# Kernel tuning notes

Measured on AMD Instinct MI355X. Metric: run time of the kernel, lower is better.

The kernel has to match this reference:

```python
import jax, jax.numpy as jnp
import numpy as np

G, IN_D, OUT_D, KQ_D = 8192, 512, 512, 128
EPS = 1e-12  # torch F.normalize default eps


def setup_inputs() -> dict:
    key = jax.random.key(0)
    ks = jax.random.split(key, 7)
    s_in = 1.0 / np.sqrt(IN_D)
    return {
        "x": jax.random.normal(ks[0], (G, IN_D), dtype=jnp.float32),
        "Wk": jax.random.uniform(ks[1], (KQ_D, IN_D), jnp.float32, -s_in, s_in),
        "bk": jax.random.uniform(ks[2], (KQ_D,), jnp.float32, -s_in, s_in),
        "Wq": jax.random.uniform(ks[3], (KQ_D, IN_D), jnp.float32, -s_in, s_in),
        "bq": jax.random.uniform(ks[4], (KQ_D,), jnp.float32, -s_in, s_in),
        "Wv": jax.random.uniform(ks[5], (OUT_D, IN_D), jnp.float32, -s_in, s_in),
        "bv": jax.random.uniform(ks[6], (OUT_D,), jnp.float32, -s_in, s_in),
    }


def reference(x, Wk, bk, Wq, bq, Wv, bv):
    # QKV projections (torch Linear: x @ W^T + b)
    k = x @ Wk.T + bk            # [g, kq]
    q = x @ Wq.T + bq            # [g, kq]
    v = x @ Wv.T + bv            # [g, outD]
    # g x g attention scores
    scores = k @ q.T             # [g, g]
    # L2-normalize each row (F.normalize with dim=-1): x / max(||x||_2, eps)
    norm = jnp.sqrt(jnp.sum(scores * scores, axis=-1, keepdims=True))
    scores_n = scores / jnp.maximum(norm, EPS)
    # value matmul + residual
    return scores_n @ v + v      # [g, outD]
```

## Files before the change

### kernel.cpp

```cpp
#include <hip/hip_runtime.h>
#include <hip/hip_bf16.h>
#include <stdint.h>

typedef __attribute__((ext_vector_type(8))) short bf16x8;
typedef __attribute__((ext_vector_type(4))) float f32x4;

__device__ __forceinline__ unsigned short f2bf(float f) {
  union { float f; uint32_t u; } v; v.f = f;
  uint32_t u = v.u;
  return (unsigned short)((u + 0x7fffu + ((u >> 16) & 1u)) >> 16);
}
__device__ __forceinline__ float bf2f(unsigned short h) {
  union { uint32_t u; float f; } v; v.u = ((uint32_t)h) << 16;
  return v.f;
}

#define GLL(g, l) __builtin_amdgcn_global_load_lds( \
    (const __attribute__((address_space(1))) void*)(g), \
    (__attribute__((address_space(3))) void*)(l), 16, 0, 0)
#define WAITV(N) asm volatile("s_waitcnt vmcnt(" #N ")" ::: "memory")
#define SFENCE() __builtin_amdgcn_sched_barrier(0)
#define RBAR()   __builtin_amdgcn_s_barrier()

__global__ void cvt_all(const float* __restrict__ x,
                        const float* __restrict__ wk, const float* __restrict__ wq,
                        const float* __restrict__ wv,
                        unsigned short* __restrict__ xb, unsigned short* __restrict__ wb) {
  const int i = (blockIdx.x * 256 + threadIdx.x) * 4;
  const float* src; unsigned short* dst; int off;
  if (i < 4194304) { src = x; dst = xb; off = i; }
  else {
    const int j = i - 4194304;
    if (j < 65536)       { src = wk; off = j; }
    else if (j < 131072) { src = wq; off = j - 65536; }
    else                 { src = wv; off = j - 131072; }
    dst = wb + (j - off);
  }
  const float4 v = *(const float4*)(src + off);
  ushort4 o; o.x = f2bf(v.x); o.y = f2bf(v.y); o.z = f2bf(v.z); o.w = f2bf(v.w);
  *(ushort4*)(dst + off) = o;
}

__global__ __launch_bounds__(512, 2) void qkv_gemm(
    const unsigned short* __restrict__ xb, const unsigned short* __restrict__ wb,
    const float* __restrict__ pbk, const float* __restrict__ pbq, const float* __restrict__ pbv,
    unsigned short* __restrict__ kb, unsigned short* __restrict__ qtb,
    unsigned short* __restrict__ vb, unsigned short* __restrict__ vtb)
{
  __shared__ unsigned short Alds[2][128 * 64];
  __shared__ unsigned short Blds[2][192 * 64];
  const int tid = threadIdx.x;
  const int lane = tid & 63;
  const int wid = tid >> 6;
  const int wm = wid >> 2, wn = wid & 3;
  const int wg = blockIdx.x;
  const int s = (wg & 7) * 32 + (wg >> 3);
  const int m0 = (s & 63) * 128;
  const int n0 = (s >> 6) * 192;
  const int l15 = lane & 15, l4 = lane >> 4;

  f32x4 acc[4][3] = {};

  auto stage = [&](int b, int kt) {
    const int k0 = kt * 64;
    #pragma unroll
    for (int p = 0; p < 2; ++p) {
      const int e = p * 512 + tid;
      const int row = e >> 3;
      const int cs = (e & 7) ^ (row & 7);
      GLL(xb + (size_t)(m0 + row) * 512 + k0 + cs * 8, &Alds[b][(p * 512 + (tid & ~63)) * 8]);
    }
    #pragma unroll
    for (int p = 0; p < 3; ++p) {
      const int e = p * 512 + tid;
      const int row = e >> 3;
      const int cs = (e & 7) ^ (row & 7);
      GLL(wb + (size_t)(n0 + row) * 512 + k0 + cs * 8, &Blds[b][(p * 512 + (tid & ~63)) * 8]);
    }
  };

  stage(0, 0);
  stage(1, 1);

  for (int kt = 0; kt < 8; ++kt) {
    const int cur = kt & 1;
    if (kt < 7) { WAITV(5); } else { WAITV(0); }
    RBAR();
    SFENCE();
    #pragma unroll
    for (int kk = 0; kk < 2; ++kk) {
      bf16x8 af[4], bfv[3];
      const int c = kk * 4 + l4;
      #pragma unroll
      for (int i = 0; i < 4; ++i) {
        const int ra = wm * 64 + i * 16 + l15;
        af[i] = *(const bf16x8*)(&Alds[cur][ra * 64 + ((c ^ (ra & 7)) * 8)]);
      }
      #pragma unroll
      for (int j = 0; j < 3; ++j) {
        const int rb = wn * 48 + j * 16 + l15;
        bfv[j] = *(const bf16x8*)(&Blds[cur][rb * 64 + ((c ^ (rb & 7)) * 8)]);
      }
      #pragma unroll
      for (int i = 0; i < 4; ++i)
        #pragma unroll
        for (int j = 0; j < 3; ++j)
          acc[i][j] = __builtin_amdgcn_mfma_f32_16x16x32_bf16(af[i], bfv[j], acc[i][j], 0, 0, 0);
    }
    SFENCE();
    RBAR();
    if (kt < 6) stage(cur, kt + 2);
  }

  #pragma unroll
  for (int i = 0; i < 4; ++i) {
    #pragma unroll
    for (int j = 0; j < 3; ++j) {
      const int rbase = m0 + wm * 64 + i * 16 + l4 * 4;
      const int c = n0 + wn * 48 + j * 16 + l15;
      const float bias = (c < 128) ? pbk[c] : (c < 256) ? pbq[c - 128] : pbv[c - 256];
      unsigned short o[4];
      #pragma unroll
      for (int r = 0; r < 4; ++r) o[r] = f2bf(acc[i][j][r] + bias);
      if (c < 128) {
        #pragma unroll
        for (int r = 0; r < 4; ++r) kb[(size_t)(rbase + r) * 128 + c] = o[r];
      } else if (c < 256) {
        ushort4 t; t.x = o[0]; t.y = o[1]; t.z = o[2]; t.w = o[3];
        *(ushort4*)(qtb + (size_t)(c - 128) * 8192 + rbase) = t;
      } else {
        const int vcol = c - 256;
        #pragma unroll
        for (int r = 0; r < 4; ++r) vb[(size_t)(rbase + r) * 512 + vcol] = o[r];
        ushort4 t; t.x = o[0]; t.y = o[1]; t.z = o[2]; t.w = o[3];
        *(ushort4*)(vtb + (size_t)vcol * 8192 + rbase) = t;
      }
    }
  }
}

__global__ __launch_bounds__(512) void gh_gemm(
    const unsigned short* __restrict__ qtb, const unsigned short* __restrict__ vtb,
    unsigned short* __restrict__ pb)
{
  __shared__ unsigned short Alds[2][128 * 64];
  __shared__ unsigned short Blds[2][80 * 64];
  const int tid = threadIdx.x, lane = tid & 63, wid = tid >> 6;
  const int l15 = lane & 15, l4 = lane >> 4;
  const int kc = blockIdx.x, nq = blockIdx.y;
  const int g0 = kc * 256;
  const int m0 = wid * 16;

  f32x4 acc[5] = {};

  auto stage = [&](int b, int st) {
    const int gs = g0 + st * 64;
    #pragma unroll
    for (int p = 0; p < 2; ++p) {
      const int e = p * 512 + tid;
      const int row = e >> 3;
      const int cs = (e & 7) ^ (row & 7);
      GLL(qtb + (size_t)row * 8192 + gs + cs * 8, &Alds[b][(p * 512 + (tid & ~63)) * 8]);
    }
    {
      const int row = tid >> 3;
      const int cglob = nq * 80 + row;
      const unsigned short* src = (cglob < 128) ? (qtb + (size_t)cglob * 8192)
                                                : (vtb + (size_t)(cglob - 128) * 8192);
      const int cs = (tid & 7) ^ (row & 7);
      GLL(src + gs + cs * 8, &Blds[b][(tid & ~63) * 8]);
    }
    if (tid < 128) {
      const int e = 512 + tid;
      const int row = e >> 3;
      const int cglob = nq * 80 + row;
      const unsigned short* src = (cglob < 128) ? (qtb + (size_t)cglob * 8192)
                                                : (vtb + (size_t)(cglob - 128) * 8192);
      const int cs = (e & 7) ^ (row & 7);
      GLL(src + gs + cs * 8, &Blds[b][(512 + (tid & ~63)) * 8]);
    }
  };

  stage(0, 0);
  stage(1, 1);

  for (int st = 0; st < 4; ++st) {
    const int cur = st & 1;
    if (st < 3) { WAITV(3); } else { WAITV(0); }
    RBAR();
    SFENCE();
    #pragma unroll
    for (int ks = 0; ks < 2; ++ks) {
      const int ra = m0 + l15;
      const int ca = ks * 4 + l4;
      const bf16x8 af = *(const bf16x8*)(&Alds[cur][ra * 64 + ((ca ^ (ra & 7)) * 8)]);
      #pragma unroll
      for (int nf = 0; nf < 5; ++nf) {
        const int rb = nf * 16 + l15;
        const bf16x8 bf = *(const bf16x8*)(&Blds[cur][rb * 64 + ((ca ^ (rb & 7)) * 8)]);
        acc[nf] = __builtin_amdgcn_mfma_f32_16x16x32_bf16(af, bf, acc[nf], 0, 0, 0);
      }
    }
    SFENCE();
    RBAR();
    if (st < 2) stage(cur, st + 2);
  }

  #pragma unroll
  for (int nf = 0; nf < 5; ++nf) {
    const int col = nq * 80 + nf * 16 + l15;
    #pragma unroll
    for (int r = 0; r < 4; ++r) {
      const int row = m0 + l4 * 4 + r;
      pb[((size_t)kc * 128 + row) * 640 + col] = f2bf(acc[nf][r]);
    }
  }
}

__global__ void gh_finalize(const unsigned short* __restrict__ pb,
                            unsigned short* __restrict__ Gb, unsigned short* __restrict__ Hbt) {
  const int idx = blockIdx.x * 256 + threadIdx.x;
  float s = 0.f;
  #pragma unroll
  for (int p = 0; p < 32; ++p) s += bf2f(pb[(size_t)p * 81920 + idx]);
  const int m = idx / 640, c = idx % 640;
  if (c < 128) Gb[m * 128 + c] = f2bf(s);
  else         Hbt[(size_t)(c - 128) * 128 + m] = f2bf(s);
}

__global__ __launch_bounds__(512) void tnorm_uv(
    const unsigned short* __restrict__ kb, const unsigned short* __restrict__ Gb,
    const unsigned short* __restrict__ Hbt, const unsigned short* __restrict__ vb,
    float* __restrict__ out)
{
  __shared__ float ssq_part[8][16];
  __shared__ float rnorm_lds[16];
  const int tid = threadIdx.x, lane = tid & 63, wid = tid >> 6;
  const int l15 = lane & 15, l4 = lane >> 4;
  const int rowbase = blockIdx.x * 16;

  bf16x8 af[4];
  #pragma unroll
  for (int ks = 0; ks < 4; ++ks)
    af[ks] = *(const bf16x8*)(kb + (size_t)(rowbase + l15) * 128 + ks * 32 + l4 * 8);

  f32x4 tac = {};
  #pragma unroll
  for (int ks = 0; ks < 4; ++ks) {
    const bf16x8 bf = *(const bf16x8*)(Gb + (size_t)(wid * 16 + l15) * 128 + ks * 32 + l4 * 8);
    tac = __builtin_amdgcn_mfma_f32_16x16x32_bf16(af[ks], bf, tac, 0, 0, 0);
  }
  float ssq[4];
  #pragma unroll
  for (int r = 0; r < 4; ++r) {
    const int row = rowbase + l4 * 4 + r;
    ssq[r] = tac[r] * bf2f(kb[(size_t)row * 128 + wid * 16 + l15]);
  }
  #pragma unroll
  for (int d = 1; d < 16; d <<= 1)
    #pragma unroll
    for (int r = 0; r < 4; ++r) ssq[r] += __shfl_xor(ssq[r], d);
  if (l15 == 0) {
    #pragma unroll
    for (int r = 0; r < 4; ++r) ssq_part[wid][l4 * 4 + r] = ssq[r];
  }

  f32x4 acc[4] = {};
  #pragma unroll
  for (int ks = 0; ks < 4; ++ks) {
    #pragma unroll
    for (int nf = 0; nf < 4; ++nf) {
      const int col = wid * 64 + nf * 16 + l15;
      const bf16x8 bf = *(const bf16x8*)(Hbt + (size_t)col * 128 + ks * 32 + l4 * 8);
      acc[nf] = __builtin_amdgcn_mfma_f32_16x16x32_bf16(af[ks], bf, acc[nf], 0, 0, 0);
    }
  }
  float vres[4][4];
  #pragma unroll
  for (int nf = 0; nf < 4; ++nf) {
    const int col = wid * 64 + nf * 16 + l15;
    #pragma unroll
    for (int r = 0; r < 4; ++r)
      vres[nf][r] = bf2f(vb[(size_t)(rowbase + l4 * 4 + r) * 512 + col]);
  }

  __syncthreads();
  if (tid < 16) {
    float s = 0.f;
    #pragma unroll
    for (int w = 0; w < 8; ++w) s += ssq_part[w][tid];
    rnorm_lds[tid] = 1.0f / fmaxf(sqrtf(s), 1e-12f);
  }
  __syncthreads();

  float rn[4];
  #pragma unroll
  for (int r = 0; r < 4; ++r) rn[r] = rnorm_lds[l4 * 4 + r];

  #pragma unroll
  for (int nf = 0; nf < 4; ++nf) {
    const int col = wid * 64 + nf * 16 + l15;
    #pragma unroll
    for (int r = 0; r < 4; ++r) {
      const int row = rowbase + l4 * 4 + r;
      out[(size_t)row * 512 + col] = acc[nf][r] * rn[r] + vres[nf][r];
    }
  }
}

extern "C" void kernel_launch(void* const* d_in, const int* in_sizes, int n_in,
                              void* d_out, int out_size, void* d_ws, size_t ws_size,
                              hipStream_t stream) {
  const float* x  = (const float*)d_in[0];
  const float* Wk = (const float*)d_in[1];
  const float* bk = (const float*)d_in[2];
  const float* Wq = (const float*)d_in[3];
  const float* bq = (const float*)d_in[4];
  const float* Wv = (const float*)d_in[5];
  const float* bv = (const float*)d_in[6];
  float* out = (float*)d_out;

  char* ws = (char*)d_ws;
  unsigned short* xb   = (unsigned short*)(ws);
  unsigned short* wb   = (unsigned short*)(ws + 8388608);
  unsigned short* kb   = (unsigned short*)(ws + 9175040);
  unsigned short* vb   = (unsigned short*)(ws + 11272192);
  unsigned short* vtb  = (unsigned short*)(ws + 19660800);
  unsigned short* qtb  = (unsigned short*)(ws + 28049408);
  unsigned short* pb   = (unsigned short*)(ws + 30146560);
  unsigned short* Gb   = (unsigned short*)(ws + 35389440);
  unsigned short* Hbt  = (unsigned short*)(ws + 35422208);

  cvt_all<<<4480, 256, 0, stream>>>(x, Wk, Wq, Wv, xb, wb);
  qkv_gemm<<<256, 512, 0, stream>>>(xb, wb, bk, bq, bv, kb, qtb, vb, vtb);
  gh_gemm<<<dim3(32, 8), 512, 0, stream>>>(qtb, vtb, pb);
  gh_finalize<<<320, 256, 0, stream>>>(pb, Gb, Hbt);
  tnorm_uv<<<512, 512, 0, stream>>>(kb, Gb, Hbt, vb, out);
}
```

Measured before the change: 54.99 us.

## Retile QKV GEMM to 256-thread blocks and stage H into LDS

The QKV projection GEMM moves from 512-thread 128x192 tiles to 256-thread 128x96 tiles, doubling the grid and changing the XCD-aware block mapping. The final normalize-and-multiply kernel now handles 32 rows per block and loads the full 512x128 H^T matrix plus the K tile into swizzled LDS with async global-to-LDS loads, so each block reuses H^T from LDS instead of reading it from global memory per 16-row block. The aim is to cut redundant global traffic and improve occupancy balance. The trade-off is a large LDS footprint (about 136 KB) that limits tnorm_uv to one block per CU, plus an initial load latency per block.

After: 58.79 us. 1.07x slower.

```diff
diff --git a/kernel.cpp b/kernel.cpp
--- a/kernel.cpp
+++ b/kernel.cpp
@@ -41,22 +41,22 @@
   *(ushort4*)(dst + off) = o;
 }
 
-__global__ __launch_bounds__(512, 2) void qkv_gemm(
+__global__ __launch_bounds__(256, 2) void qkv_gemm(
     const unsigned short* __restrict__ xb, const unsigned short* __restrict__ wb,
     const float* __restrict__ pbk, const float* __restrict__ pbq, const float* __restrict__ pbv,
     unsigned short* __restrict__ kb, unsigned short* __restrict__ qtb,
     unsigned short* __restrict__ vb, unsigned short* __restrict__ vtb)
 {
   __shared__ unsigned short Alds[2][128 * 64];
-  __shared__ unsigned short Blds[2][192 * 64];
+  __shared__ unsigned short Blds[2][96 * 64];
   const int tid = threadIdx.x;
   const int lane = tid & 63;
   const int wid = tid >> 6;
-  const int wm = wid >> 2, wn = wid & 3;
+  const int wm = wid >> 1, wn = wid & 1;
   const int wg = blockIdx.x;
-  const int s = (wg & 7) * 32 + (wg >> 3);
-  const int m0 = (s & 63) * 128;
-  const int n0 = (s >> 6) * 192;
+  const int xcd = wg & 7, i6 = wg >> 3;
+  const int m0 = (xcd * 8 + (i6 & 7)) * 128;
+  const int n0 = (i6 >> 3) * 96;
   const int l15 = lane & 15, l4 = lane >> 4;
 
   f32x4 acc[4][3] = {};
@@ -64,18 +64,18 @@
   auto stage = [&](int b, int kt) {
     const int k0 = kt * 64;
     #pragma unroll
-    for (int p = 0; p < 2; ++p) {
-      const int e = p * 512 + tid;
+    for (int p = 0; p < 4; ++p) {
+      const int e = p * 256 + tid;
       const int row = e >> 3;
       const int cs = (e & 7) ^ (row & 7);
-      GLL(xb + (size_t)(m0 + row) * 512 + k0 + cs * 8, &Alds[b][(p * 512 + (tid & ~63)) * 8]);
+      GLL(xb + (size_t)(m0 + row) * 512 + k0 + cs * 8, &Alds[b][(p * 256 + (tid & ~63)) * 8]);
     }
     #pragma unroll
     for (int p = 0; p < 3; ++p) {
-      const int e = p * 512 + tid;
+      const int e = p * 256 + tid;
       const int row = e >> 3;
       const int cs = (e & 7) ^ (row & 7);
-      GLL(wb + (size_t)(n0 + row) * 512 + k0 + cs * 8, &Blds[b][(p * 512 + (tid & ~63)) * 8]);
+      GLL(wb + (size_t)(n0 + row) * 512 + k0 + cs * 8, &Blds[b][(p * 256 + (tid & ~63)) * 8]);
     }
   };
 
@@ -84,7 +84,7 @@
 
   for (int kt = 0; kt < 8; ++kt) {
     const int cur = kt & 1;
-    if (kt < 7) { WAITV(5); } else { WAITV(0); }
+    if (kt < 7) { WAITV(7); } else { WAITV(0); }
     RBAR();
     SFENCE();
     #pragma unroll
@@ -228,81 +228,115 @@
   else         Hbt[(size_t)(c - 128) * 128 + m] = f2bf(s);
 }
 
-__global__ __launch_bounds__(512) void tnorm_uv(
+__global__ __launch_bounds__(512, 1) void tnorm_uv(
     const unsigned short* __restrict__ kb, const unsigned short* __restrict__ Gb,
     const unsigned short* __restrict__ Hbt, const unsigned short* __restrict__ vb,
     float* __restrict__ out)
 {
-  __shared__ float ssq_part[8][16];
-  __shared__ float rnorm_lds[16];
+  __shared__ unsigned short Hlds[512 * 128];
+  __shared__ unsigned short Kld[32 * 128];
+  __shared__ float ssq_part[8][32];
+  __shared__ float rnorm_lds[32];
   const int tid = threadIdx.x, lane = tid & 63, wid = tid >> 6;
   const int l15 = lane & 15, l4 = lane >> 4;
-  const int rowbase = blockIdx.x * 16;
-
-  bf16x8 af[4];
-  #pragma unroll
-  for (int ks = 0; ks < 4; ++ks)
-    af[ks] = *(const bf16x8*)(kb + (size_t)(rowbase + l15) * 128 + ks * 32 + l4 * 8);
-
-  f32x4 tac = {};
+  const int m0 = blockIdx.x * 32;
+  const int mf = wid & 1, nq = wid >> 1;
+
+  {
+    const int row = tid >> 4, ch = tid & 15;
+    GLL(kb + (size_t)(m0 + row) * 128 + (ch ^ ((row & 7) << 1)) * 8,
+        &Kld[(tid & ~63) * 8]);
+  }
+  #pragma unroll
+  for (int p = 0; p < 16; ++p) {
+    const int e = p * 512 + tid;
+    const int row = e >> 4, ch = e & 15;
+    GLL(Hbt + (size_t)row * 128 + (ch ^ ((row & 7) << 1)) * 8,
+        &Hlds[(p * 512 + (tid & ~63)) * 8]);
+  }
+  WAITV(16);
+  __syncthreads();
+
+  bf16x8 afh[2][4];
+  #pragma unroll
+  for (int h = 0; h < 2; ++h)
+    #pragma unroll
+    for (int ks = 0; ks < 4; ++ks) {
+      const int row = h * 16 + l15, ci = ks * 4 + l4;
+      afh[h][ks] = *(const bf16x8*)((const char*)Kld + row * 256 + ((ci ^ ((row & 7) << 1)) * 16));
+    }
+  f32x4 tach[2] = {};
   #pragma unroll
   for (int ks = 0; ks < 4; ++ks) {
-    const bf16x8 bf = *(const bf16x8*)(Gb + (size_t)(wid * 16 + l15) * 128 + ks * 32 + l4 * 8);
-    tac = __builtin_amdgcn_mfma_f32_16x16x32_bf16(af[ks], bf, tac, 0, 0, 0);
-  }
-  float ssq[4];
-  #pragma unroll
-  for (int r = 0; r < 4; ++r) {
-    const int row = rowbase + l4 * 4 + r;
-    ssq[r] = tac[r] * bf2f(kb[(size_t)row * 128 + wid * 16 + l15]);
-  }
-  #pragma unroll
-  for (int d = 1; d < 16; d <<= 1)
-    #pragma unroll
-    for (int r = 0; r < 4; ++r) ssq[r] += __shfl_xor(ssq[r], d);
-  if (l15 == 0) {
-    #pragma unroll
-    for (int r = 0; r < 4; ++r) ssq_part[wid][l4 * 4 + r] = ssq[r];
-  }
-
-  f32x4 acc[4] = {};
-  #pragma unroll
-  for (int ks = 0; ks < 4; ++ks) {
-    #pragma unroll
-    for (int nf = 0; nf < 4; ++nf) {
-      const int col = wid * 64 + nf * 16 + l15;
-      const bf16x8 bf = *(const bf16x8*)(Hbt + (size_t)col * 128 + ks * 32 + l4 * 8);
-      acc[nf] = __builtin_amdgcn_mfma_f32_16x16x32_bf16(af[ks], bf, acc[nf], 0, 0, 0);
-    }
-  }
-  float vres[4][4];
-  #pragma unroll
-  for (int nf = 0; nf < 4; ++nf) {
-    const int col = wid * 64 + nf * 16 + l15;
-    #pragma unroll
-    for (int r = 0; r < 4; ++r)
-      vres[nf][r] = bf2f(vb[(size_t)(rowbase + l4 * 4 + r) * 512 + col]);
-  }
-
+    const bf16x8 bfG = *(const bf16x8*)(Gb + (size_t)(wid * 16 + l15) * 128 + ks * 32 + l4 * 8);
+    #pragma unroll
+    for (int h = 0; h < 2; ++h)
+      tach[h] = __builtin_amdgcn_mfma_f32_16x16x32_bf16(afh[h][ks], bfG, tach[h], 0, 0, 0);
+  }
+  #pragma unroll
+  for (int h = 0; h < 2; ++h) {
+    float ssq[4];
+    #pragma unroll
+    for (int r = 0; r < 4; ++r) {
+      const int row = h * 16 + l4 * 4 + r;
+      const int col = wid * 16 + l15;
+      const unsigned short kv = *(const unsigned short*)((const char*)Kld + row * 256 +
+          (((col >> 3) ^ ((row & 7) << 1)) * 16) + (col & 7) * 2);
+      ssq[r] = tach[h][r] * bf2f(kv);
+    }
+    #pragma unroll
+    for (int d = 1; d < 16; d <<= 1)
+      #pragma unroll
+      for (int r = 0; r < 4; ++r) ssq[r] += __shfl_xor(ssq[r], d);
+    if (l15 == 0) {
+      #pragma unroll
+      for (int r = 0; r < 4; ++r) ssq_part[wid][h * 16 + l4 * 4 + r] = ssq[r];
+    }
+  }
+
+  WAITV(0);
   __syncthreads();
-  if (tid < 16) {
+
+  if (tid < 32) {
     float s = 0.f;
     #pragma unroll
     for (int w = 0; w < 8; ++w) s += ssq_part[w][tid];
     rnorm_lds[tid] = 1.0f / fmaxf(sqrtf(s), 1e-12f);
   }
+
+  f32x4 acc[8] = {};
+  #pragma unroll
+  for (int ks = 0; ks < 4; ++ks) {
+    #pragma unroll
+    for (int nf = 0; nf < 8; ++nf) {
+      const int hrow = nq * 128 + nf * 16 + l15;
+      const int ci = ks * 4 + l4;
+      const bf16x8 bf = *(const bf16x8*)((const char*)Hlds + hrow * 256 +
+                                         ((ci ^ ((hrow & 7) << 1)) * 16));
+      acc[nf] = __builtin_amdgcn_mfma_f32_16x16x32_bf16(afh[mf][ks], bf, acc[nf], 0, 0, 0);
+    }
+  }
+  float vres[8][4];
+  #pragma unroll
+  for (int nf = 0; nf < 8; ++nf) {
+    const int col = nq * 128 + nf * 16 + l15;
+    #pragma unroll
+    for (int r = 0; r < 4; ++r)
+      vres[nf][r] = bf2f(vb[(size_t)(m0 + mf * 16 + l4 * 4 + r) * 512 + col]);
+  }
+
   __syncthreads();
 
   float rn[4];
   #pragma unroll
-  for (int r = 0; r < 4; ++r) rn[r] = rnorm_lds[l4 * 4 + r];
-
-  #pragma unroll
-  for (int nf = 0; nf < 4; ++nf) {
-    const int col = wid * 64 + nf * 16 + l15;
+  for (int r = 0; r < 4; ++r) rn[r] = rnorm_lds[mf * 16 + l4 * 4 + r];
+
+  #pragma unroll
+  for (int nf = 0; nf < 8; ++nf) {
+    const int col = nq * 128 + nf * 16 + l15;
     #pragma unroll
     for (int r = 0; r < 4; ++r) {
-      const int row = rowbase + l4 * 4 + r;
+      const int row = m0 + mf * 16 + l4 * 4 + r;
       out[(size_t)row * 512 + col] = acc[nf][r] * rn[r] + vres[nf][r];
     }
   }
@@ -332,8 +366,8 @@
   unsigned short* Hbt  = (unsigned short*)(ws + 35422208);
 
   cvt_all<<<4480, 256, 0, stream>>>(x, Wk, Wq, Wv, xb, wb);
-  qkv_gemm<<<256, 512, 0, stream>>>(xb, wb, bk, bq, bv, kb, qtb, vb, vtb);
+  qkv_gemm<<<512, 256, 0, stream>>>(xb, wb, bk, bq, bv, kb, qtb, vb, vtb);
   gh_gemm<<<dim3(32, 8), 512, 0, stream>>>(qtb, vtb, pb);
   gh_finalize<<<320, 256, 0, stream>>>(pb, Gb, Hbt);
-  tnorm_uv<<<512, 512, 0, stream>>>(kb, Gb, Hbt, vb, out);
-}
+  tnorm_uv<<<256, 512, 0, stream>>>(kb, Gb, Hbt, vb, out);
+}
```
